# Kernel tuning notes

Measured on AMD Instinct MI355X. Metric: run time of the kernel, lower is better.

Reference implementation:

```python
import jax, jax.numpy as jnp
import numpy as np
import math

B, S, D, H = 4, 1024, 512, 8
HD = D // H
HID = 4 * D


def clinear(xr, xi, lm, ph, bm=None, bp=None):
    # magnitude-phase parameterized complex linear: W = exp(lm) * e^{i*ph}
    mag = jnp.exp(lm)
    wr = mag * jnp.cos(ph)
    wi = mag * jnp.sin(ph)
    r = xr @ wr.T - xi @ wi.T
    i = xr @ wi.T + xi @ wr.T
    if bm is not None:
        r = r + bm * jnp.cos(bp)
        i = i + bm * jnp.sin(bp)
    return r, i


def cln(xr, xi, gr, gi, br, bi, eps=1e-6):
    mr = xr.mean(-1, keepdims=True)
    mi = xi.mean(-1, keepdims=True)
    cr, ci = xr - mr, xi - mi
    var = (cr * cr + ci * ci).mean(-1, keepdims=True)
    inv = 1.0 / jnp.sqrt(var + eps)
    nr, ni = cr * inv, ci * inv
    return nr * gr - ni * gi + br, nr * gi + ni * gr + bi


def rotate_half(x):
    h = x.shape[-1] // 2
    return jnp.concatenate([-x[..., h:], x[..., :h]], axis=-1)


def split_heads(x):  # (B,S,D) -> (B,H,S,HD)
    return x.reshape(B, S, H, HD).transpose(0, 2, 1, 3)


def merge_heads(x):  # (B,H,S,HD) -> (B,S,D)
    return x.transpose(0, 2, 1, 3).reshape(B, S, D)


def setup_inputs() -> dict:
    key = jax.random.key(0)
    ks = iter(jax.random.split(key, 64))

    def lin(o_f, i_f):
        lm = jax.random.normal(next(ks), (o_f, i_f)) * 0.1 - 0.5 * math.log(i_f)
        ph = jax.random.uniform(next(ks), (o_f, i_f), minval=-math.pi, maxval=math.pi)
        return lm.astype(jnp.float32), ph.astype(jnp.float32)

    inp = {}
    inp['x_real'] = jax.random.normal(next(ks), (B, S, D), dtype=jnp.float32)
    inp['x_imag'] = jax.random.normal(next(ks), (B, S, D), dtype=jnp.float32)
    inp['ln1_gr'] = jnp.ones(D); inp['ln1_gi'] = jnp.zeros(D)
    inp['ln1_br'] = jnp.zeros(D); inp['ln1_bi'] = jnp.zeros(D)
    for nm in ['q', 'k', 'v', 'o']:
        lm, ph = lin(D, D)
        inp[nm + '_lm'] = lm; inp[nm + '_ph'] = ph
        inp[nm + '_bm'] = jnp.zeros(D); inp[nm + '_bp'] = jnp.zeros(D)
    inp['ln2_gr'] = jnp.ones(D); inp['ln2_gi'] = jnp.zeros(D)
    inp['ln2_br'] = jnp.zeros(D); inp['ln2_bi'] = jnp.zeros(D)
    inp['gate_lm'], inp['gate_ph'] = lin(HID, D)
    inp['up_lm'], inp['up_ph'] = lin(HID, D)
    inp['down_lm'], inp['down_ph'] = lin(D, HID)
    return inp


def reference(x_real, x_imag, ln1_gr, ln1_gi, ln1_br, ln1_bi,
              q_lm, q_ph, q_bm, q_bp, k_lm, k_ph, k_bm, k_bp,
              v_lm, v_ph, v_bm, v_bp, o_lm, o_ph, o_bm, o_bp,
              ln2_gr, ln2_gi, ln2_br, ln2_bi,
              gate_lm, gate_ph, up_lm, up_ph, down_lm, down_ph):
    # --- pre-attention complex LayerNorm ---
    hr, hi = cln(x_real, x_imag, ln1_gr, ln1_gi, ln1_br, ln1_bi)

    # --- complex QKV projections ---
    qr, qi = clinear(hr, hi, q_lm, q_ph, q_bm, q_bp)
    kr, ki = clinear(hr, hi, k_lm, k_ph, k_bm, k_bp)
    vr, vi = clinear(hr, hi, v_lm, v_ph, v_bm, v_bp)
    qr, qi = split_heads(qr), split_heads(qi)
    kr, ki = split_heads(kr), split_heads(ki)
    vr, vi = split_heads(vr), split_heads(vi)

    # --- complex RoPE (same real rotation applied to real & imag parts) ---
    pos = jnp.arange(S, dtype=jnp.float32)
    inv_freq = 1.0 / (10000.0 ** (jnp.arange(0, HD, 2, dtype=jnp.float32) / HD))
    freqs = pos[:, None] * inv_freq[None, :]          # (S, HD/2)
    cos = jnp.concatenate([jnp.cos(freqs)] * 2, -1)[None, None]  # (1,1,S,HD)
    sin = jnp.concatenate([jnp.sin(freqs)] * 2, -1)[None, None]
    rot = lambda x: x * cos + rotate_half(x) * sin
    qr, qi, kr, ki = rot(qr), rot(qi), rot(kr), rot(ki)

    # --- Hermitian attention: Re(q . conj(k)) = qr.kr + qi.ki ---
    scale = 1.0 / math.sqrt(HD)
    scores = (jnp.einsum('bhqd,bhkd->bhqk', qr, kr)
              + jnp.einsum('bhqd,bhkd->bhqk', qi, ki)) * scale
    causal = jnp.tril(jnp.ones((S, S), dtype=bool))
    scores = jnp.where(causal, scores, jnp.float32(-1e9))
    attn = jax.nn.softmax(scores, axis=-1)            # real-valued weights
    ar = jnp.einsum('bhqk,bhkd->bhqd', attn, vr)
    ai = jnp.einsum('bhqk,bhkd->bhqd', attn, vi)
    ar, ai = merge_heads(ar), merge_heads(ai)
    ar, ai = clinear(ar, ai, o_lm, o_ph, o_bm, o_bp)

    # --- residual + LN2 ---
    res_r, res_i = x_real + ar, x_imag + ai
    hr, hi = cln(res_r, res_i, ln2_gr, ln2_gi, ln2_br, ln2_bi)

    # --- complex gated FFN (SwiGLU-style, complex gating) ---
    gr_, gi_ = clinear(hr, hi, gate_lm, gate_ph)
    s = jax.nn.sigmoid(jnp.sqrt(gr_ * gr_ + gi_ * gi_))  # sigmoid(|gate|)
    gar, gai = gr_ * s, gi_ * s
    ur, ui = clinear(hr, hi, up_lm, up_ph)
    hid_r = gar * ur - gai * ui
    hid_i = gar * ui + gai * ur
    dr, di = clinear(hid_r, hid_i, down_lm, down_ph)

    out_r = res_r + dr
    out_i = res_i + di
    return jnp.stack([out_r, out_i], axis=0)  # (2, B, S, D)
```

## Files before the change

kernel.cpp:

```cpp
#include <hip/hip_runtime.h>
#include <math.h>

#define kB 4
#define kS 1024
#define kD 512
#define kH 8
#define kHD 64
#define kHID 2048
#define kNT (kB * kS)
#define kBSD (kNT * kD)

typedef __attribute__((ext_vector_type(8))) short bf16x8;
typedef __attribute__((ext_vector_type(4))) float f32x4;

#define AS1 __attribute__((address_space(1)))
#define AS3 __attribute__((address_space(3)))

__device__ __forceinline__ float bf2f(unsigned short u) {
  return __uint_as_float(((unsigned int)u) << 16);
}
__device__ __forceinline__ unsigned short f2bf(float f) {
  unsigned int u = __float_as_uint(f);
  u += 0x7fffu + ((u >> 16) & 1u);
  return (unsigned short)(u >> 16);
}
__device__ __forceinline__ unsigned int pack2(unsigned short a, unsigned short b) {
  return (unsigned)a | ((unsigned)b << 16);
}

#define BARC() do { asm volatile("" ::: "memory"); __builtin_amdgcn_s_barrier(); asm volatile("" ::: "memory"); } while (0)

__global__ __launch_bounds__(256) void build_wA_kernel(
    const float* __restrict__ qlm, const float* __restrict__ qph,
    const float* __restrict__ klm, const float* __restrict__ kph,
    const float* __restrict__ vlm, const float* __restrict__ vph,
    const float* __restrict__ olm, const float* __restrict__ oph,
    const float* __restrict__ qbm, const float* __restrict__ qbp,
    const float* __restrict__ kbm, const float* __restrict__ kbp,
    const float* __restrict__ vbm, const float* __restrict__ vbp,
    const float* __restrict__ obm, const float* __restrict__ obp,
    const float* __restrict__ xr, const float* __restrict__ xi,
    const float* __restrict__ g_r, const float* __restrict__ g_i,
    const float* __restrict__ b_r, const float* __restrict__ b_i,
    unsigned short* __restrict__ Wqkv, unsigned short* __restrict__ Wo,
    float* __restrict__ qkvBias, float* __restrict__ oBias,
    unsigned short* __restrict__ H) {
  int bx = blockIdx.x;
  if (bx >= 4104) {
    int w = threadIdx.x >> 6, lane = threadIdx.x & 63;
    int t = (bx - 4104) * 4 + w;
    int d0 = lane * 8;
    const float* xrt = xr + (size_t)t * 512 + d0;
    const float* xit = xi + (size_t)t * 512 + d0;
    float4 a0 = *(const float4*)&xrt[0];
    float4 a1 = *(const float4*)&xrt[4];
    float4 c0 = *(const float4*)&xit[0];
    float4 c1 = *(const float4*)&xit[4];
    float s1 = a0.x + a0.y + a0.z + a0.w + a1.x + a1.y + a1.z + a1.w;
    float s2 = c0.x + c0.y + c0.z + c0.w + c1.x + c1.y + c1.z + c1.w;
#pragma unroll
    for (int off = 1; off < 64; off <<= 1) {
      s1 += __shfl_xor(s1, off);
      s2 += __shfl_xor(s2, off);
    }
    float mr = s1 * (1.f / kD), mi = s2 * (1.f / kD);
    float ar[8] = {a0.x, a0.y, a0.z, a0.w, a1.x, a1.y, a1.z, a1.w};
    float ai[8] = {c0.x, c0.y, c0.z, c0.w, c1.x, c1.y, c1.z, c1.w};
    float v = 0.f;
#pragma unroll
    for (int e = 0; e < 8; e++) {
      float cr = ar[e] - mr, ci = ai[e] - mi;
      v += cr * cr + ci * ci;
    }
#pragma unroll
    for (int off = 1; off < 64; off <<= 1) v += __shfl_xor(v, off);
    float inv = rsqrtf(v * (1.f / kD) + 1e-6f);
    unsigned short pr[8], pi[8];
#pragma unroll
    for (int e = 0; e < 8; e++) {
      float nr = (ar[e] - mr) * inv;
      float ni = (ai[e] - mi) * inv;
      pr[e] = f2bf(nr * g_r[d0 + e] - ni * g_i[d0 + e] + b_r[d0 + e]);
      pi[e] = f2bf(nr * g_i[d0 + e] + ni * g_r[d0 + e] + b_i[d0 + e]);
    }
    unsigned short* ot = H + (size_t)t * 1024 + d0;
    *(bf16x8*)&ot[0] = *(const bf16x8*)pr;
    *(bf16x8*)&ot[512] = *(const bf16x8*)pi;
    return;
  }
  if (bx >= 4096) {
    int gid = (bx - 4096) * 256 + threadIdx.x;
    int seg = gid >> 9, m = gid & 511;
    const float* bm = seg == 0 ? qbm : seg == 1 ? kbm : seg == 2 ? vbm : obm;
    const float* bp = seg == 0 ? qbp : seg == 1 ? kbp : seg == 2 ? vbp : obp;
    float s, c;
    __sincosf(bp[m], &s, &c);
    float br = bm[m] * c, bi = bm[m] * s;
    if (seg < 3) {
      int h = m >> 6, d = m & 63;
      qkvBias[seg * 1024 + h * 128 + d] = br;
      qkvBias[seg * 1024 + h * 128 + 64 + d] = bi;
    } else {
      oBias[m] = br;
      oBias[512 + m] = bi;
    }
    return;
  }
  int gid = bx * 256 + threadIdx.x;
  int seg = gid >> 18;
  int id = gid & 262143;
  const float* lm = seg == 0 ? qlm : seg == 1 ? klm : seg == 2 ? vlm : olm;
  const float* ph = seg == 0 ? qph : seg == 1 ? kph : seg == 2 ? vph : oph;
  float mm = __expf(lm[id]);
  float s, c;
  __sincosf(ph[id], &s, &c);
  float wr = mm * c, wi = mm * s;
  int m = id >> 9, k = id & 511;
  if (seg < 3) {
    int h = m >> 6, d = m & 63;
    size_t rowR = (size_t)seg * 1024 + h * 128 + d;
    size_t rowI = rowR + 64;
    Wqkv[rowR * 1024 + k] = f2bf(wr);
    Wqkv[rowR * 1024 + 512 + k] = f2bf(-wi);
    Wqkv[rowI * 1024 + k] = f2bf(wi);
    Wqkv[rowI * 1024 + 512 + k] = f2bf(wr);
  } else {
    Wo[(size_t)m * 1024 + k] = f2bf(wr);
    Wo[(size_t)m * 1024 + 512 + k] = f2bf(-wi);
    Wo[(size_t)(512 + m) * 1024 + k] = f2bf(wi);
    Wo[(size_t)(512 + m) * 1024 + 512 + k] = f2bf(wr);
  }
}

__global__ __launch_bounds__(256) void build_wB_kernel(
    const float* __restrict__ glm, const float* __restrict__ gph,
    const float* __restrict__ ulm, const float* __restrict__ uph,
    const float* __restrict__ dlm, const float* __restrict__ dph,
    unsigned short* __restrict__ Wgu, unsigned short* __restrict__ Wd) {
  int gid = blockIdx.x * 256 + threadIdx.x;
  int seg = gid >> 19;
  int id0 = (gid & 524287) * 2;
  const float* lm = seg == 0 ? glm : seg == 1 ? ulm : dlm;
  const float* ph = seg == 0 ? gph : seg == 1 ? uph : dph;
  float2 lm2 = *(const float2*)&lm[id0];
  float2 ph2 = *(const float2*)&ph[id0];
  float m0 = __expf(lm2.x), m1 = __expf(lm2.y);
  float s0, c0, s1, c1;
  __sincosf(ph2.x, &s0, &c0);
  __sincosf(ph2.y, &s1, &c1);
  float wr0 = m0 * c0, wi0 = m0 * s0;
  float wr1 = m1 * c1, wi1 = m1 * s1;
  if (seg < 2) {
    int T = id0 >> 9, k = id0 & 511;
    size_t base = (size_t)(T >> 4) * 64 + (T & 15);
    size_t rR = base + (seg * 2 + 0) * 16;
    size_t rI = base + (seg * 2 + 1) * 16;
    *(unsigned int*)&Wgu[rR * 1024 + k] = pack2(f2bf(wr0), f2bf(wr1));
    *(unsigned int*)&Wgu[rR * 1024 + 512 + k] = pack2(f2bf(-wi0), f2bf(-wi1));
    *(unsigned int*)&Wgu[rI * 1024 + k] = pack2(f2bf(wi0), f2bf(wi1));
    *(unsigned int*)&Wgu[rI * 1024 + 512 + k] = pack2(f2bf(wr0), f2bf(wr1));
  } else {
    int m = id0 >> 11, j = id0 & 2047;
    ushort4 a;
    a.x = f2bf(wr0); a.y = f2bf(-wi0); a.z = f2bf(wr1); a.w = f2bf(-wi1);
    *(ushort4*)&Wd[(size_t)m * 4096 + 2 * j] = a;
    ushort4 b;
    b.x = f2bf(wi0); b.y = f2bf(wr0); b.z = f2bf(wi1); b.w = f2bf(wr1);
    *(ushort4*)&Wd[(size_t)(512 + m) * 4096 + 2 * j] = b;
  }
}

__global__ __launch_bounds__(256) void cln_kernel(
    const float* __restrict__ xr, const float* __restrict__ xi, int stride,
    const float* __restrict__ g_r, const float* __restrict__ g_i,
    const float* __restrict__ b_r, const float* __restrict__ b_i,
    unsigned short* __restrict__ out) {
  int w = threadIdx.x >> 6, lane = threadIdx.x & 63;
  int t = blockIdx.x * 4 + w;
  int d0 = lane * 8;
  const float* xrt = xr + (size_t)t * stride + d0;
  const float* xit = xi + (size_t)t * stride + d0;
  float4 a0 = *(const float4*)&xrt[0];
  float4 a1 = *(const float4*)&xrt[4];
  float4 c0 = *(const float4*)&xit[0];
  float4 c1 = *(const float4*)&xit[4];

  float s1 = a0.x + a0.y + a0.z + a0.w + a1.x + a1.y + a1.z + a1.w;
  float s2 = c0.x + c0.y + c0.z + c0.w + c1.x + c1.y + c1.z + c1.w;
#pragma unroll
  for (int off = 1; off < 64; off <<= 1) {
    s1 += __shfl_xor(s1, off);
    s2 += __shfl_xor(s2, off);
  }
  float mr = s1 * (1.f / kD), mi = s2 * (1.f / kD);

  float ar[8] = {a0.x, a0.y, a0.z, a0.w, a1.x, a1.y, a1.z, a1.w};
  float ai[8] = {c0.x, c0.y, c0.z, c0.w, c1.x, c1.y, c1.z, c1.w};
  float v = 0.f;
#pragma unroll
  for (int e = 0; e < 8; e++) {
    float cr = ar[e] - mr, ci = ai[e] - mi;
    v += cr * cr + ci * ci;
  }
#pragma unroll
  for (int off = 1; off < 64; off <<= 1) v += __shfl_xor(v, off);
  float inv = rsqrtf(v * (1.f / kD) + 1e-6f);

  unsigned short pr[8], pi[8];
#pragma unroll
  for (int e = 0; e < 8; e++) {
    float nr = (ar[e] - mr) * inv;
    float ni = (ai[e] - mi) * inv;
    pr[e] = f2bf(nr * g_r[d0 + e] - ni * g_i[d0 + e] + b_r[d0 + e]);
    pi[e] = f2bf(nr * g_i[d0 + e] + ni * g_r[d0 + e] + b_i[d0 + e]);
  }
  unsigned short* ot = out + (size_t)t * 1024 + d0;
  *(bf16x8*)&ot[0] = *(const bf16x8*)pr;
  *(bf16x8*)&ot[512] = *(const bf16x8*)pi;
}

__global__ __launch_bounds__(256) void cgemm_mfma_kernel(
    const unsigned short* __restrict__ X, int ldx,
    const unsigned short* __restrict__ Wt, int K,
    const float* __restrict__ bias, int mode,
    unsigned short* __restrict__ outb, int ldo,
    unsigned short* __restrict__ vtb) {
  __shared__ unsigned short Sh[128 * 64 * 2];
  unsigned short* Xs = Sh;
  unsigned short* Ws = Sh + 8192;

  const int tid = threadIdx.x;
  const int w = tid >> 6;
  const int lane = tid & 63;
  const int quad = lane >> 4;
  const int l15 = lane & 15;
  const int m0 = blockIdx.x * 128;
  const int n0 = blockIdx.y * 128;
  const int wm = (w & 1) * 64;
  const int wn = (w >> 1) * 64;

  const int rsub = lane >> 3;
  const int grow = w * 32 + rsub;
  const int gcol = ((lane & 7) ^ rsub) * 8;
  const unsigned short* gx = X + (size_t)(n0 + grow) * ldx + gcol;
  const unsigned short* gw = Wt + (size_t)(m0 + grow) * K + gcol;

  const int rg = (l15 & 7);

  f32x4 acc[4][4];
#pragma unroll
  for (int i = 0; i < 4; i++)
#pragma unroll
    for (int j = 0; j < 4; j++) acc[i][j] = (f32x4){0.f, 0.f, 0.f, 0.f};

  for (int k0 = 0; k0 < K; k0 += 64) {
    __syncthreads();
#pragma unroll
    for (int t = 0; t < 4; t++) {
      __builtin_amdgcn_global_load_lds((const AS1 void*)(gx + (size_t)t * 8 * ldx + k0),
                                       (AS3 void*)&Xs[w * 2048 + t * 512], 16, 0, 0);
      __builtin_amdgcn_global_load_lds((const AS1 void*)(gw + (size_t)t * 8 * K + k0),
                                       (AS3 void*)&Ws[w * 2048 + t * 512], 16, 0, 0);
    }
    __syncthreads();

#pragma unroll
    for (int ks = 0; ks < 2; ks++) {
      const int gsel = ((ks * 4 + quad) ^ rg) * 8;
      bf16x8 af[4], bf[4];
#pragma unroll
      for (int t = 0; t < 4; t++) {
        af[t] = *(const bf16x8*)&Xs[(wn + t * 16 + l15) * 64 + gsel];
        bf[t] = *(const bf16x8*)&Ws[(wm + t * 16 + l15) * 64 + gsel];
      }
#pragma unroll
      for (int i = 0; i < 4; i++)
#pragma unroll
        for (int j = 0; j < 4; j++)
          acc[i][j] = __builtin_amdgcn_mfma_f32_16x16x32_bf16(af[i], bf[j], acc[i][j], 0, 0, 0);
    }
  }

  if (mode == 4) {
    int T = ((m0 + wm) >> 6) * 16 + l15;
#pragma unroll
    for (int i = 0; i < 4; ++i) {
      int row0 = n0 + wn + i * 16 + quad * 4;
#pragma unroll
      for (int r = 0; r < 4; ++r) {
        float gr = acc[i][0][r], gi = acc[i][1][r];
        float ur = acc[i][2][r], ui = acc[i][3][r];
        float sg = __builtin_amdgcn_rcpf(1.f + __expf(-sqrtf(gr * gr + gi * gi)));
        float gar = gr * sg, gai = gi * sg;
        unsigned int pk = pack2(f2bf(gar * ur - gai * ui), f2bf(gar * ui + gai * ur));
        *(unsigned int*)&outb[(size_t)(row0 + r) * ldo + 2 * T] = pk;
      }
    }
  } else if (mode == 3 && m0 < 2048) {
#pragma unroll
    for (int j = 0; j < 4; ++j) {
      float bv = bias[m0 + wm + j * 16 + l15];
#pragma unroll
      for (int i = 0; i < 4; ++i)
#pragma unroll
        for (int r = 0; r < 4; ++r) acc[i][j][r] += bv;
    }
    const int sbase = ((n0 + wn) & (kS - 1)) + quad * 4;
#pragma unroll
    for (int j01 = 0; j01 < 2; ++j01) {
      float fi = (float)(j01 * 16 + l15);
      float f = __expf(fi * -0.28782313662425572f);
      float c1, s1, c16, s16, cI, sI;
      __sincosf(f, &s1, &c1);
      __sincosf(16.f * f, &s16, &c16);
      __sincosf((float)sbase * f, &sI, &cI);
#pragma unroll
      for (int i = 0; i < 4; ++i) {
        float cc = cI, ss = sI;
#pragma unroll
        for (int r = 0; r < 4; ++r) {
          float x0 = acc[i][j01][r], x1 = acc[i][j01 + 2][r];
          acc[i][j01][r] = x0 * cc - x1 * ss;
          acc[i][j01 + 2][r] = x1 * cc + x0 * ss;
          float cn = cc * c1 - ss * s1;
          ss = ss * c1 + cc * s1;
          cc = cn;
        }
        float cn = cI * c16 - sI * s16;
        sI = sI * c16 + cI * s16;
        cI = cn;
      }
    }
#pragma unroll
    for (int j = 0; j < 4; ++j) {
      int col = m0 + wm + j * 16 + l15;
#pragma unroll
      for (int i = 0; i < 4; ++i) {
        int row0 = n0 + wn + i * 16 + quad * 4;
#pragma unroll
        for (int r = 0; r < 4; ++r)
          outb[(size_t)(row0 + r) * ldo + col] = f2bf(acc[i][j][r]);
      }
    }
  } else {
    unsigned short* Ts = Sh;
#pragma unroll
    for (int p = 0; p < 2; ++p) {
      __syncthreads();
      if ((w & 1) == p) {
#pragma unroll
        for (int j = 0; j < 4; ++j) {
          float bv = bias[m0 + wm + j * 16 + l15];
          int fl = j * 16 + l15;
#pragma unroll
          for (int i = 0; i < 4; ++i) {
            int tk = wn + i * 16 + quad * 4;
#pragma unroll
            for (int r = 0; r < 4; ++r)
              Ts[fl * 130 + tk + r] = f2bf(acc[i][j][r] + bv);
          }
        }
      }
      __syncthreads();
      {
        int fr = tid >> 2, seg = tid & 3;
        int f = (m0 - 2048) + p * 64 + fr;
        int hh = f >> 7, dc = f & 127;
        int bb = n0 >> 10, sbase2 = (n0 & (kS - 1)) + seg * 32;
        unsigned short* dst = &vtb[(size_t)((bb * 8 + hh) * 128 + dc) * 1024 + sbase2];
        const unsigned short* src = &Ts[fr * 130 + seg * 32];
#pragma unroll
        for (int u = 0; u < 4; u++)
          *(bf16x8*)(dst + u * 8) = *(const bf16x8*)(src + u * 8);
      }
    }
  }
}

__global__ __launch_bounds__(512, 2) void cgemm_mfma_gu256_kernel(
    const unsigned short* __restrict__ X, int ldx,
    const unsigned short* __restrict__ Wt, int K,
    unsigned short* __restrict__ outb, int ldo) {
  __shared__ unsigned short Sh[65536];

  const int tid = threadIdx.x;
  const int w = tid >> 6;
  const int lane = tid & 63;
  const int quad = lane >> 4;
  const int l15 = lane & 15;
  const int m0 = blockIdx.x * 256;
  const int n0 = blockIdx.y * 256;
  const int wfeat = w & 1;
  const int wtok = w >> 1;

  const int srow = lane >> 3;
  const int sgran = ((lane & 7) ^ srow) * 8;
  const unsigned short* gA = X + (size_t)(n0 + w * 32 + srow) * ldx + sgran;
  const unsigned short* gB = Wt + (size_t)(m0 + w * 32 + srow) * K + sgran;

  f32x4 acc[4][8];
#pragma unroll
  for (int i = 0; i < 4; i++)
#pragma unroll
    for (int j = 0; j < 8; j++) acc[i][j] = (f32x4){0.f, 0.f, 0.f, 0.f};

  auto stage_tile = [&](int kt, int bsel) {
    const int k0 = kt * 64;
    unsigned short* dA = &Sh[bsel * 32768 + w * 2048];
    unsigned short* dB = &Sh[bsel * 32768 + 16384 + w * 2048];
#pragma unroll
    for (int u = 0; u < 4; ++u) {
      __builtin_amdgcn_global_load_lds((const AS1 void*)(gA + (size_t)u * 8 * ldx + k0),
                                       (AS3 void*)(dA + u * 512), 16, 0, 0);
      __builtin_amdgcn_global_load_lds((const AS1 void*)(gB + (size_t)u * 8 * K + k0),
                                       (AS3 void*)(dB + u * 512), 16, 0, 0);
    }
  };

  auto compute_tile = [&](const unsigned short* As, const unsigned short* Bs) {
    bf16x8 af[4][2];
#pragma unroll
    for (int i = 0; i < 4; ++i)
#pragma unroll
      for (int ks = 0; ks < 2; ++ks)
        af[i][ks] = *(const bf16x8*)&As[(wtok * 64 + i * 16 + l15) * 64 +
                                        (((ks * 4 + quad) ^ (l15 & 7)) * 8)];
#pragma unroll
    for (int jp = 0; jp < 4; ++jp) {
      bf16x8 bq[2][2];
#pragma unroll
      for (int jj = 0; jj < 2; ++jj)
#pragma unroll
        for (int ks = 0; ks < 2; ++ks)
          bq[jj][ks] = *(const bf16x8*)&Bs[(wfeat * 128 + (jp * 2 + jj) * 16 + l15) * 64 +
                                           (((ks * 4 + quad) ^ (l15 & 7)) * 8)];
      __builtin_amdgcn_s_setprio(1);
#pragma unroll
      for (int i = 0; i < 4; ++i)
#pragma unroll
        for (int jj = 0; jj < 2; ++jj) {
          const int j = jp * 2 + jj;
          acc[i][j] = __builtin_amdgcn_mfma_f32_16x16x32_bf16(af[i][0], bq[jj][0], acc[i][j], 0, 0, 0);
          acc[i][j] = __builtin_amdgcn_mfma_f32_16x16x32_bf16(af[i][1], bq[jj][1], acc[i][j], 0, 0, 0);
        }
      __builtin_amdgcn_s_setprio(0);
    }
  };

  const int nt = K >> 6;
  stage_tile(0, 0);
  for (int t = 0; t < nt; t += 2) {
    if (t + 1 < nt) {
      stage_tile(t + 1, 1);
      asm volatile("s_waitcnt vmcnt(8)" ::: "memory");
    } else {
      asm volatile("s_waitcnt vmcnt(0)" ::: "memory");
    }
    __builtin_amdgcn_s_barrier();
    asm volatile("" ::: "memory");
    compute_tile(&Sh[0], &Sh[16384]);
    asm volatile("" ::: "memory");
    __builtin_amdgcn_s_barrier();

    if (t + 2 < nt) {
      stage_tile(t + 2, 0);
      asm volatile("s_waitcnt vmcnt(8)" ::: "memory");
    } else {
      asm volatile("s_waitcnt vmcnt(0)" ::: "memory");
    }
    __builtin_amdgcn_s_barrier();
    asm volatile("" ::: "memory");
    compute_tile(&Sh[32768], &Sh[32768 + 16384]);
    asm volatile("" ::: "memory");
    __builtin_amdgcn_s_barrier();
  }

#pragma unroll
  for (int i = 0; i < 4; ++i) {
    int row0 = n0 + wtok * 64 + i * 16 + quad * 4;
#pragma unroll
    for (int jh = 0; jh < 2; ++jh) {
      int T = ((m0 + wfeat * 128 + jh * 64) >> 6) * 16 + l15;
#pragma unroll
      for (int r = 0; r < 4; ++r) {
        float gr = acc[i][jh * 4 + 0][r], gi = acc[i][jh * 4 + 1][r];
        float ur = acc[i][jh * 4 + 2][r], ui = acc[i][jh * 4 + 3][r];
        float sg = __builtin_amdgcn_rcpf(1.f + __expf(-sqrtf(gr * gr + gi * gi)));
        float gar = gr * sg, gai = gi * sg;
        unsigned int pk = pack2(f2bf(gar * ur - gai * ui), f2bf(gar * ui + gai * ur));
        *(unsigned int*)&outb[(size_t)(row0 + r) * ldo + 2 * T] = pk;
      }
    }
  }
}

__global__ __launch_bounds__(256) void cgemm_mfma_n64_kernel(
    const unsigned short* __restrict__ X, int ldx,
    const unsigned short* __restrict__ Wt, int K,
    const float* __restrict__ bias, int mode,
    const float* __restrict__ resr, const float* __restrict__ resi,
    float* __restrict__ outf) {
  __shared__ unsigned short Sh[24576];

  const int tid = threadIdx.x;
  const int w = tid >> 6;
  const int lane = tid & 63;
  const int quad = lane >> 4;
  const int l15 = lane & 15;
  const int m0 = blockIdx.x * 128;
  const int n0 = blockIdx.y * 64;
  const int wm = (w & 1) * 64;
  const int wn = (w >> 1) * 32;
  const int swz = l15 & 7;

  const int srow = lane >> 3;
  const int sgran = ((lane & 7) ^ srow) * 8;
  const unsigned short* gX = X + (size_t)(n0 + w * 16 + srow) * ldx + sgran;
  const unsigned short* gW = Wt + (size_t)(m0 + w * 32 + srow) * K + sgran;

  f32x4 acc[2][4];
#pragma unroll
  for (int i = 0; i < 2; i++)
#pragma unroll
    for (int j = 0; j < 4; j++) acc[i][j] = (f32x4){0.f, 0.f, 0.f, 0.f};

  auto stage_tile = [&](int kt, int bsel) {
    const int k0 = kt * 64;
    unsigned short* dX = &Sh[bsel * 12288 + w * 1024];
    unsigned short* dW = &Sh[bsel * 12288 + 4096 + w * 2048];
#pragma unroll
    for (int u = 0; u < 2; ++u)
      __builtin_amdgcn_global_load_lds((const AS1 void*)(gX + (size_t)u * 8 * ldx + k0),
                                       (AS3 void*)(dX + u * 512), 16, 0, 0);
#pragma unroll
    for (int u = 0; u < 4; ++u)
      __builtin_amdgcn_global_load_lds((const AS1 void*)(gW + (size_t)u * 8 * K + k0),
                                       (AS3 void*)(dW + u * 512), 16, 0, 0);
  };

  const int nt = K >> 6;
  stage_tile(0, 0);
  for (int t = 0; t < nt; ++t) {
    if (t + 1 < nt) {
      stage_tile(t + 1, (t + 1) & 1);
      asm volatile("s_waitcnt vmcnt(6)" ::: "memory");
    } else {
      asm volatile("s_waitcnt vmcnt(0)" ::: "memory");
    }
    BARC();
    const unsigned short* Xs = &Sh[(t & 1) * 12288];
    const unsigned short* Ws = &Sh[(t & 1) * 12288 + 4096];
#pragma unroll
    for (int ks = 0; ks < 2; ++ks) {
      const int gsel = ((ks * 4 + quad) ^ swz) * 8;
      bf16x8 af[2], bf[4];
#pragma unroll
      for (int t2 = 0; t2 < 2; ++t2)
        af[t2] = *(const bf16x8*)&Xs[(wn + t2 * 16 + l15) * 64 + gsel];
#pragma unroll
      for (int t2 = 0; t2 < 4; ++t2)
        bf[t2] = *(const bf16x8*)&Ws[(wm + t2 * 16 + l15) * 64 + gsel];
#pragma unroll
      for (int i = 0; i < 2; i++)
#pragma unroll
        for (int j = 0; j < 4; j++)
          acc[i][j] = __builtin_amdgcn_mfma_f32_16x16x32_bf16(af[i], bf[j], acc[i][j], 0, 0, 0);
    }
    BARC();
  }

#pragma unroll
  for (int j = 0; j < 4; ++j) {
    int col = m0 + wm + j * 16 + l15;
    float bv = bias ? bias[col] : 0.f;
#pragma unroll
    for (int i = 0; i < 2; ++i) {
      int row0 = n0 + wn + i * 16 + quad * 4;
#pragma unroll
      for (int r = 0; r < 4; ++r) {
        int row = row0 + r;
        float val = acc[i][j][r] + bv;
        if (mode == 1) {
          float xres = (col < 512) ? resr[(size_t)row * 512 + col]
                                   : resi[(size_t)row * 512 + col - 512];
          outf[(size_t)row * 1024 + col] = val + xres;
        } else {
          float rv = resr[(size_t)row * 1024 + col] + val;
          size_t dd = (col < 512) ? ((size_t)row * 512 + col)
                                  : ((size_t)kBSD + (size_t)row * 512 + (col - 512));
          outf[dd] = rv;
        }
      }
    }
  }
}

__global__ __launch_bounds__(256) void attn_mfma_kernel(
    const unsigned short* __restrict__ qkv,
    const unsigned short* __restrict__ vt,
    unsigned short* __restrict__ out) {
  __shared__ unsigned short Ks[64 * 136];
  __shared__ unsigned short Vs[128 * 72];
  __shared__ unsigned short Ps[4 * 16 * 72];

  const int tid = threadIdx.x;
  const int w = tid >> 6;
  const int lane = tid & 63;
  const int quad = lane >> 4;
  const int l15 = lane & 15;

  int bid = blockIdx.x;
  int second = bid >> 8;
  int u = bid & 255;
  int t_ = u & 15;
  const int qt = second ? (15 - t_) : t_;
  const int h = (u >> 4) & 7;
  const int b = second * 2 + (u >> 7);
  const int q0 = qt * 64;
  const int wrow0 = q0 + w * 16;

  bf16x8 qa[4];
  {
    size_t base = (size_t)(b * kS + wrow0 + l15) * 3072 + h * 128;
#pragma unroll
    for (int ks = 0; ks < 4; ks++)
      qa[ks] = *(const bf16x8*)&qkv[base + ks * 32 + quad * 8];
  }

  f32x4 oacc[8];
#pragma unroll
  for (int dt = 0; dt < 8; dt++) oacc[dt] = (f32x4){0.f, 0.f, 0.f, 0.f};
  float m_r[4] = {-1e30f, -1e30f, -1e30f, -1e30f};
  float l_r[4] = {0.f, 0.f, 0.f, 0.f};

  const int nkt = qt + 1;
  const float cexp = 0.1803368801f;

  const unsigned short* gkbase = qkv + 1024 + h * 128;
  const unsigned short* gvbase = vt + (size_t)((b * 8 + h) * 128) * 1024;

  for (int kt = 0; kt < nkt; ++kt) {
    const int k0 = kt * 64;
    __syncthreads();
    {
      const unsigned short* gk = gkbase + (size_t)(b * kS + k0) * 3072;
      int ch = tid * 4;
#pragma unroll
      for (int u2 = 0; u2 < 4; u2++) {
        int r = (ch + u2) >> 4, cc = ((ch + u2) & 15) * 8;
        *(bf16x8*)&Ks[r * 136 + cc] = *(const bf16x8*)&gk[(size_t)r * 3072 + cc];
      }
#pragma unroll
      for (int u2 = 0; u2 < 4; u2++) {
        int vr = (ch + u2) >> 3, vc = ((ch + u2) & 7) * 8;
        *(bf16x8*)&Vs[vr * 72 + vc] = *(const bf16x8*)&gvbase[(size_t)vr * 1024 + k0 + vc];
      }
    }
    __syncthreads();

    f32x4 s[4];
#pragma unroll
    for (int ns = 0; ns < 4; ns++) {
      s[ns] = (f32x4){0.f, 0.f, 0.f, 0.f};
#pragma unroll
      for (int ks = 0; ks < 4; ks++) {
        bf16x8 kb = *(const bf16x8*)&Ks[(ns * 16 + l15) * 136 + ks * 32 + quad * 8];
        s[ns] = __builtin_amdgcn_mfma_f32_16x16x32_bf16(qa[ks], kb, s[ns], 0, 0, 0);
      }
    }

    if (k0 + 63 > wrow0) {
#pragma unroll
      for (int r = 0; r < 4; r++) {
        int qrow = wrow0 + quad * 4 + r;
#pragma unroll
        for (int ns = 0; ns < 4; ns++)
          if (k0 + ns * 16 + l15 > qrow) s[ns][r] = -1e30f;
      }
    }

    float alpha[4];
#pragma unroll
    for (int r = 0; r < 4; r++) {
      float mx = fmaxf(fmaxf(s[0][r], s[1][r]), fmaxf(s[2][r], s[3][r]));
      mx = fmaxf(mx, __shfl_xor(mx, 1));
      mx = fmaxf(mx, __shfl_xor(mx, 2));
      mx = fmaxf(mx, __shfl_xor(mx, 4));
      mx = fmaxf(mx, __shfl_xor(mx, 8));
      float mn = fmaxf(m_r[r], mx);
      float al = exp2f((m_r[r] - mn) * cexp);
      m_r[r] = mn;
      float rs = 0.f;
#pragma unroll
      for (int ns = 0; ns < 4; ns++) {
        float p = exp2f((s[ns][r] - mn) * cexp);
        s[ns][r] = p;
        rs += p;
      }
      rs += __shfl_xor(rs, 1);
      rs += __shfl_xor(rs, 2);
      rs += __shfl_xor(rs, 4);
      rs += __shfl_xor(rs, 8);
      l_r[r] = l_r[r] * al + rs;
      alpha[r] = al;
    }

#pragma unroll
    for (int dt = 0; dt < 8; dt++)
#pragma unroll
      for (int r = 0; r < 4; r++) oacc[dt][r] *= alpha[r];

    unsigned short* pw = &Ps[w * 1152];
#pragma unroll
    for (int r = 0; r < 4; r++) {
      int q = quad * 4 + r;
#pragma unroll
      for (int ns = 0; ns < 4; ns++)
        pw[q * 72 + ns * 16 + l15] = f2bf(s[ns][r]);
    }
    bf16x8 pa0 = *(const bf16x8*)&pw[l15 * 72 + quad * 8];
    bf16x8 pa1 = *(const bf16x8*)&pw[l15 * 72 + 32 + quad * 8];

#pragma unroll
    for (int dt = 0; dt < 8; dt++) {
      bf16x8 vb0 = *(const bf16x8*)&Vs[(dt * 16 + l15) * 72 + quad * 8];
      bf16x8 vb1 = *(const bf16x8*)&Vs[(dt * 16 + l15) * 72 + 32 + quad * 8];
      oacc[dt] = __builtin_amdgcn_mfma_f32_16x16x32_bf16(pa0, vb0, oacc[dt], 0, 0, 0);
      oacc[dt] = __builtin_amdgcn_mfma_f32_16x16x32_bf16(pa1, vb1, oacc[dt], 0, 0, 0);
    }
  }

  float inv[4];
#pragma unroll
  for (int r = 0; r < 4; r++) inv[r] = __builtin_amdgcn_rcpf(l_r[r]);
#pragma unroll
  for (int dt = 0; dt < 8; dt++) {
    int dcat = dt * 16 + l15;
    int col = (dcat < 64) ? (h * 64 + dcat) : (512 + h * 64 + dcat - 64);
#pragma unroll
    for (int r = 0; r < 4; r++) {
      int tok = b * kS + wrow0 + quad * 4 + r;
      out[(size_t)tok * 1024 + col] = f2bf(oacc[dt][r] * inv[r]);
    }
  }
}

extern "C" void kernel_launch(void* const* d_in, const int* in_sizes, int n_in,
                              void* d_out, int out_size, void* d_ws, size_t ws_size,
                              hipStream_t stream) {
  const float* x_real = (const float*)d_in[0];
  const float* x_imag = (const float*)d_in[1];
  const float* ln1_gr = (const float*)d_in[2];
  const float* ln1_gi = (const float*)d_in[3];
  const float* ln1_br = (const float*)d_in[4];
  const float* ln1_bi = (const float*)d_in[5];
  const float* q_lm = (const float*)d_in[6];
  const float* q_ph = (const float*)d_in[7];
  const float* q_bm = (const float*)d_in[8];
  const float* q_bp = (const float*)d_in[9];
  const float* k_lm = (const float*)d_in[10];
  const float* k_ph = (const float*)d_in[11];
  const float* k_bm = (const float*)d_in[12];
  const float* k_bp = (const float*)d_in[13];
  const float* v_lm = (const float*)d_in[14];
  const float* v_ph = (const float*)d_in[15];
  const float* v_bm = (const float*)d_in[16];
  const float* v_bp = (const float*)d_in[17];
  const float* o_lm = (const float*)d_in[18];
  const float* o_ph = (const float*)d_in[19];
  const float* o_bm = (const float*)d_in[20];
  const float* o_bp = (const float*)d_in[21];
  const float* ln2_gr = (const float*)d_in[22];
  const float* ln2_gi = (const float*)d_in[23];
  const float* ln2_br = (const float*)d_in[24];
  const float* ln2_bi = (const float*)d_in[25];
  const float* gate_lm = (const float*)d_in[26];
  const float* gate_ph = (const float*)d_in[27];
  const float* up_lm = (const float*)d_in[28];
  const float* up_ph = (const float*)d_in[29];
  const float* down_lm = (const float*)d_in[30];
  const float* down_ph = (const float*)d_in[31];

  char* wsb = (char*)d_ws;
  unsigned short* Wqkv = (unsigned short*)(wsb + 0);
  unsigned short* Wo   = (unsigned short*)(wsb + 6291456);
  unsigned short* Wgu  = (unsigned short*)(wsb + 8388608);
  unsigned short* Wd   = (unsigned short*)(wsb + 25165824);
  float* qkvBias = (float*)(wsb + 33554432);
  float* oBias   = (float*)(wsb + 33566720);
  float* res     = (float*)(wsb + 33570816);
  unsigned short* H = (unsigned short*)(wsb + 50348032);
  char* big = wsb + 58736640;
  unsigned short* qkv     = (unsigned short*)big;
  unsigned short* attnout = (unsigned short*)(big + 25165824);
  unsigned short* vtb     = (unsigned short*)(big + 33554432);
  unsigned short* hid     = (unsigned short*)big;

  float* outf = (float*)d_out;

  build_wA_kernel<<<5128, 256, 0, stream>>>(q_lm, q_ph, k_lm, k_ph, v_lm, v_ph,
                                            o_lm, o_ph, q_bm, q_bp, k_bm, k_bp,
                                            v_bm, v_bp, o_bm, o_bp,
                                            x_real, x_imag, ln1_gr, ln1_gi,
                                            ln1_br, ln1_bi,
                                            Wqkv, Wo, qkvBias, oBias, H);
  build_wB_kernel<<<6144, 256, 0, stream>>>(gate_lm, gate_ph, up_lm, up_ph,
                                            down_lm, down_ph, Wgu, Wd);

  {
    dim3 g(3072 / 128, kNT / 128);
    cgemm_mfma_kernel<<<g, 256, 0, stream>>>(H, 1024, Wqkv, 1024, qkvBias, 3, qkv, 3072, vtb);
  }

  attn_mfma_kernel<<<kB * kH * (kS / 64), 256, 0, stream>>>(qkv, vtb, attnout);

  {
    dim3 g(1024 / 128, kNT / 64);
    cgemm_mfma_n64_kernel<<<g, 256, 0, stream>>>(attnout, 1024, Wo, 1024, oBias, 1,
                                                 x_real, x_imag, res);
  }

  cln_kernel<<<kNT / 4, 256, 0, stream>>>(res, res + 512, 1024, ln2_gr, ln2_gi, ln2_br, ln2_bi, H);

  {
    dim3 g(8192 / 256, kNT / 256);
    cgemm_mfma_gu256_kernel<<<g, 512, 0, stream>>>(H, 1024, Wgu, 1024, hid, 4096);
  }

  {
    dim3 g(1024 / 128, kNT / 64);
    cgemm_mfma_n64_kernel<<<g, 256, 0, stream>>>(hid, 4096, Wd, 4096, nullptr, 2,
                                                 res, nullptr, outf);
  }
}
```

Before: 388.3 us.

## Interleave chunked global-to-LDS staging with MFMA phases in gate/up GEMM

Restructures the gate/up fused GEMM main loop so that global_load_lds staging is split into four half-tile chunks. Each chunk is issued between LDS fragment reads and an MFMA quad, with barriers around each quad. The aim is to spread memory traffic across the compute phases and keep the next tiles in flight, so LDS refills overlap with MFMA work instead of arriving as one burst per tile. The cost is more barriers per k-tile and tighter vmcnt bookkeeping, which could serialize warps or create hazards if the counts are off.

```diff
diff --git a/kernel.cpp b/kernel.cpp
--- a/kernel.cpp
+++ b/kernel.cpp
@@ -392,11 +392,10 @@
   const int n0 = blockIdx.y * 256;
   const int wfeat = w & 1;
   const int wtok = w >> 1;
+  const int swz = l15 & 7;
 
   const int srow = lane >> 3;
   const int sgran = ((lane & 7) ^ srow) * 8;
-  const unsigned short* gA = X + (size_t)(n0 + w * 32 + srow) * ldx + sgran;
-  const unsigned short* gB = Wt + (size_t)(m0 + w * 32 + srow) * K + sgran;
 
   f32x4 acc[4][8];
 #pragma unroll
@@ -404,75 +403,90 @@
 #pragma unroll
     for (int j = 0; j < 8; j++) acc[i][j] = (f32x4){0.f, 0.f, 0.f, 0.f};
 
-  auto stage_tile = [&](int kt, int bsel) {
+  auto stage_chunk = [&](int kt, int which) {
     const int k0 = kt * 64;
-    unsigned short* dA = &Sh[bsel * 32768 + w * 2048];
-    unsigned short* dB = &Sh[bsel * 32768 + 16384 + w * 2048];
-#pragma unroll
-    for (int u = 0; u < 4; ++u) {
-      __builtin_amdgcn_global_load_lds((const AS1 void*)(gA + (size_t)u * 8 * ldx + k0),
-                                       (AS3 void*)(dA + u * 512), 16, 0, 0);
-      __builtin_amdgcn_global_load_lds((const AS1 void*)(gB + (size_t)u * 8 * K + k0),
-                                       (AS3 void*)(dB + u * 512), 16, 0, 0);
+    const int bsel = kt & 1;
+    const int half = which & 1;
+    if (which < 2) {
+      const unsigned short* g =
+          X + (size_t)(n0 + half * 128 + w * 16 + srow) * ldx + k0 + sgran;
+      unsigned short* d = &Sh[bsel * 32768 + (half * 128 + w * 16) * 64];
+#pragma unroll
+      for (int u = 0; u < 2; ++u)
+        __builtin_amdgcn_global_load_lds((const AS1 void*)(g + (size_t)u * 8 * ldx),
+                                         (AS3 void*)(d + u * 512), 16, 0, 0);
+    } else {
+      const unsigned short* g =
+          Wt + (size_t)(m0 + half * 128 + w * 16 + srow) * K + k0 + sgran;
+      unsigned short* d = &Sh[bsel * 32768 + 16384 + (half * 128 + w * 16) * 64];
+#pragma unroll
+      for (int u = 0; u < 2; ++u)
+        __builtin_amdgcn_global_load_lds((const AS1 void*)(g + (size_t)u * 8 * K),
+                                         (AS3 void*)(d + u * 512), 16, 0, 0);
     }
   };
 
-  auto compute_tile = [&](const unsigned short* As, const unsigned short* Bs) {
-    bf16x8 af[4][2];
+  bf16x8 af[4][2];
+  bf16x8 bq[4];
+
+  auto read_bq = [&](const unsigned short* Bs, int ks, int jh) {
+#pragma unroll
+    for (int jj = 0; jj < 4; ++jj)
+      bq[jj] = *(const bf16x8*)&Bs[(wfeat * 128 + jh * 64 + jj * 16 + l15) * 64 +
+                                   (((ks * 4 + quad) ^ swz) * 8)];
+  };
+
+  auto mfma_quad = [&](int ks, int jh) {
+    __builtin_amdgcn_s_barrier();
+    __builtin_amdgcn_s_setprio(1);
+#pragma unroll
+    for (int i = 0; i < 4; ++i)
+#pragma unroll
+      for (int jj = 0; jj < 4; ++jj)
+        acc[i][jh * 4 + jj] = __builtin_amdgcn_mfma_f32_16x16x32_bf16(
+            af[i][ks], bq[jj], acc[i][jh * 4 + jj], 0, 0, 0);
+    __builtin_amdgcn_s_setprio(0);
+    __builtin_amdgcn_s_barrier();
+  };
+
+  const int nt = K >> 6;
+  stage_chunk(0, 0); stage_chunk(0, 1); stage_chunk(0, 2); stage_chunk(0, 3);
+  stage_chunk(1, 0); stage_chunk(1, 1);
+  asm volatile("s_waitcnt vmcnt(4)" ::: "memory");
+  __builtin_amdgcn_s_barrier();
+
+  for (int t = 0; t < nt; ++t) {
+    const unsigned short* As = &Sh[(t & 1) * 32768];
+    const unsigned short* Bs = &Sh[(t & 1) * 32768 + 16384];
+
 #pragma unroll
     for (int i = 0; i < 4; ++i)
 #pragma unroll
       for (int ks = 0; ks < 2; ++ks)
         af[i][ks] = *(const bf16x8*)&As[(wtok * 64 + i * 16 + l15) * 64 +
-                                        (((ks * 4 + quad) ^ (l15 & 7)) * 8)];
-#pragma unroll
-    for (int jp = 0; jp < 4; ++jp) {
-      bf16x8 bq[2][2];
-#pragma unroll
-      for (int jj = 0; jj < 2; ++jj)
-#pragma unroll
-        for (int ks = 0; ks < 2; ++ks)
-          bq[jj][ks] = *(const bf16x8*)&Bs[(wfeat * 128 + (jp * 2 + jj) * 16 + l15) * 64 +
-                                           (((ks * 4 + quad) ^ (l15 & 7)) * 8)];
-      __builtin_amdgcn_s_setprio(1);
-#pragma unroll
-      for (int i = 0; i < 4; ++i)
-#pragma unroll
-        for (int jj = 0; jj < 2; ++jj) {
-          const int j = jp * 2 + jj;
-          acc[i][j] = __builtin_amdgcn_mfma_f32_16x16x32_bf16(af[i][0], bq[jj][0], acc[i][j], 0, 0, 0);
-          acc[i][j] = __builtin_amdgcn_mfma_f32_16x16x32_bf16(af[i][1], bq[jj][1], acc[i][j], 0, 0, 0);
-        }
-      __builtin_amdgcn_s_setprio(0);
-    }
-  };
-
-  const int nt = K >> 6;
-  stage_tile(0, 0);
-  for (int t = 0; t < nt; t += 2) {
-    if (t + 1 < nt) {
-      stage_tile(t + 1, 1);
-      asm volatile("s_waitcnt vmcnt(8)" ::: "memory");
+                                        (((ks * 4 + quad) ^ swz) * 8)];
+    read_bq(Bs, 0, 0);
+    if (t + 1 < nt) stage_chunk(t + 1, 2);
+    mfma_quad(0, 0);
+#pragma unroll
+    for (int i = 0; i < 4; ++i) asm volatile("" :: "v"(af[i][1]));
+
+    read_bq(Bs, 0, 1);
+    if (t + 1 < nt) stage_chunk(t + 1, 3);
+    mfma_quad(0, 1);
+
+    read_bq(Bs, 1, 0);
+    if (t + 2 < nt) stage_chunk(t + 2, 0);
+    mfma_quad(1, 0);
+
+    read_bq(Bs, 1, 1);
+    if (t + 2 < nt) {
+      stage_chunk(t + 2, 1);
+      asm volatile("s_waitcnt vmcnt(4)" ::: "memory");
     } else {
       asm volatile("s_waitcnt vmcnt(0)" ::: "memory");
     }
-    __builtin_amdgcn_s_barrier();
-    asm volatile("" ::: "memory");
-    compute_tile(&Sh[0], &Sh[16384]);
-    asm volatile("" ::: "memory");
-    __builtin_amdgcn_s_barrier();
-
-    if (t + 2 < nt) {
-      stage_tile(t + 2, 0);
-      asm volatile("s_waitcnt vmcnt(8)" ::: "memory");
-    } else {
-      asm volatile("s_waitcnt vmcnt(0)" ::: "memory");
-    }
-    __builtin_amdgcn_s_barrier();
-    asm volatile("" ::: "memory");
-    compute_tile(&Sh[32768], &Sh[32768 + 16384]);
-    asm volatile("" ::: "memory");
-    __builtin_amdgcn_s_barrier();
+    mfma_quad(1, 1);
   }
 
 #pragma unroll
```

Result: no change. 385.7 us (-0.7%).

## Shrink gate/up GEMM tile to 256x128 with BK=32 and higher occupancy

Applied to the files above, without the earlier changes.

The fused gate/up complex GEMM moves from a 256x256 tile with K-step 64 and two-tile unrolled double buffering to a 256x128 tile with K-step 32, single-iteration ping-pong buffering and a new XOR swizzle. LDS use drops from 128KB to 48KB and launch bounds ask for 4 blocks per CU, doubling the grid. This aims at better occupancy and latency hiding, at the cost of less operand reuse per tile, more barriers per unit of K, and more redundant loads of X.

```diff
diff --git a/kernel.cpp b/kernel.cpp
--- a/kernel.cpp
+++ b/kernel.cpp
@@ -377,119 +377,89 @@
   }
 }
 
-__global__ __launch_bounds__(512, 2) void cgemm_mfma_gu256_kernel(
+__global__ __launch_bounds__(512, 4) void cgemm_mfma_gu256_kernel(
     const unsigned short* __restrict__ X, int ldx,
     const unsigned short* __restrict__ Wt, int K,
     unsigned short* __restrict__ outb, int ldo) {
-  __shared__ unsigned short Sh[65536];
+  __shared__ unsigned short Sh[24576];
 
   const int tid = threadIdx.x;
   const int w = tid >> 6;
   const int lane = tid & 63;
   const int quad = lane >> 4;
   const int l15 = lane & 15;
-  const int m0 = blockIdx.x * 256;
+  const int m0 = blockIdx.x * 128;
   const int n0 = blockIdx.y * 256;
   const int wfeat = w & 1;
   const int wtok = w >> 1;
 
-  const int srow = lane >> 3;
-  const int sgran = ((lane & 7) ^ srow) * 8;
-  const unsigned short* gA = X + (size_t)(n0 + w * 32 + srow) * ldx + sgran;
-  const unsigned short* gB = Wt + (size_t)(m0 + w * 32 + srow) * K + sgran;
-
-  f32x4 acc[4][8];
+  const int srow = lane >> 2;
+  const int sgran = ((lane & 3) ^ ((srow >> 1) & 3)) * 8;
+  const unsigned short* gX = X + (size_t)(n0 + w * 32 + srow) * ldx + sgran;
+  const unsigned short* gW = Wt + (size_t)(m0 + w * 16 + srow) * K + sgran;
+
+  f32x4 acc[4][4];
 #pragma unroll
   for (int i = 0; i < 4; i++)
 #pragma unroll
-    for (int j = 0; j < 8; j++) acc[i][j] = (f32x4){0.f, 0.f, 0.f, 0.f};
+    for (int j = 0; j < 4; j++) acc[i][j] = (f32x4){0.f, 0.f, 0.f, 0.f};
 
   auto stage_tile = [&](int kt, int bsel) {
-    const int k0 = kt * 64;
-    unsigned short* dA = &Sh[bsel * 32768 + w * 2048];
-    unsigned short* dB = &Sh[bsel * 32768 + 16384 + w * 2048];
-#pragma unroll
-    for (int u = 0; u < 4; ++u) {
-      __builtin_amdgcn_global_load_lds((const AS1 void*)(gA + (size_t)u * 8 * ldx + k0),
-                                       (AS3 void*)(dA + u * 512), 16, 0, 0);
-      __builtin_amdgcn_global_load_lds((const AS1 void*)(gB + (size_t)u * 8 * K + k0),
-                                       (AS3 void*)(dB + u * 512), 16, 0, 0);
-    }
+    const int k0 = kt * 32;
+    unsigned short* dX = &Sh[bsel * 12288 + w * 1024];
+    unsigned short* dW = &Sh[bsel * 12288 + 8192 + w * 512];
+    __builtin_amdgcn_global_load_lds((const AS1 void*)(gX + k0),
+                                     (AS3 void*)(dX), 16, 0, 0);
+    __builtin_amdgcn_global_load_lds((const AS1 void*)(gX + (size_t)16 * ldx + k0),
+                                     (AS3 void*)(dX + 512), 16, 0, 0);
+    __builtin_amdgcn_global_load_lds((const AS1 void*)(gW + k0),
+                                     (AS3 void*)(dW), 16, 0, 0);
   };
 
-  auto compute_tile = [&](const unsigned short* As, const unsigned short* Bs) {
-    bf16x8 af[4][2];
-#pragma unroll
-    for (int i = 0; i < 4; ++i)
-#pragma unroll
-      for (int ks = 0; ks < 2; ++ks)
-        af[i][ks] = *(const bf16x8*)&As[(wtok * 64 + i * 16 + l15) * 64 +
-                                        (((ks * 4 + quad) ^ (l15 & 7)) * 8)];
-#pragma unroll
-    for (int jp = 0; jp < 4; ++jp) {
-      bf16x8 bq[2][2];
-#pragma unroll
-      for (int jj = 0; jj < 2; ++jj)
-#pragma unroll
-        for (int ks = 0; ks < 2; ++ks)
-          bq[jj][ks] = *(const bf16x8*)&Bs[(wfeat * 128 + (jp * 2 + jj) * 16 + l15) * 64 +
-                                           (((ks * 4 + quad) ^ (l15 & 7)) * 8)];
-      __builtin_amdgcn_s_setprio(1);
-#pragma unroll
-      for (int i = 0; i < 4; ++i)
-#pragma unroll
-        for (int jj = 0; jj < 2; ++jj) {
-          const int j = jp * 2 + jj;
-          acc[i][j] = __builtin_amdgcn_mfma_f32_16x16x32_bf16(af[i][0], bq[jj][0], acc[i][j], 0, 0, 0);
-          acc[i][j] = __builtin_amdgcn_mfma_f32_16x16x32_bf16(af[i][1], bq[jj][1], acc[i][j], 0, 0, 0);
-        }
-      __builtin_amdgcn_s_setprio(0);
-    }
-  };
-
-  const int nt = K >> 6;
+  const int gsel = ((quad ^ ((l15 >> 1) & 3)) * 8);
+  const int aoff = (wtok * 64 + l15) * 32 + gsel;
+  const int boff = (wfeat * 64 + l15) * 32 + gsel;
+
+  const int nt = K >> 5;
   stage_tile(0, 0);
-  for (int t = 0; t < nt; t += 2) {
+  for (int t = 0; t < nt; ++t) {
     if (t + 1 < nt) {
-      stage_tile(t + 1, 1);
-      asm volatile("s_waitcnt vmcnt(8)" ::: "memory");
+      stage_tile(t + 1, (t + 1) & 1);
+      asm volatile("s_waitcnt vmcnt(3)" ::: "memory");
     } else {
       asm volatile("s_waitcnt vmcnt(0)" ::: "memory");
     }
-    __builtin_amdgcn_s_barrier();
-    asm volatile("" ::: "memory");
-    compute_tile(&Sh[0], &Sh[16384]);
-    asm volatile("" ::: "memory");
-    __builtin_amdgcn_s_barrier();
-
-    if (t + 2 < nt) {
-      stage_tile(t + 2, 0);
-      asm volatile("s_waitcnt vmcnt(8)" ::: "memory");
-    } else {
-      asm volatile("s_waitcnt vmcnt(0)" ::: "memory");
-    }
-    __builtin_amdgcn_s_barrier();
-    asm volatile("" ::: "memory");
-    compute_tile(&Sh[32768], &Sh[32768 + 16384]);
-    asm volatile("" ::: "memory");
-    __builtin_amdgcn_s_barrier();
-  }
-
+    BARC();
+    const unsigned short* As = &Sh[(t & 1) * 12288];
+    const unsigned short* Ws = &Sh[(t & 1) * 12288 + 8192];
+    bf16x8 af[4];
+#pragma unroll
+    for (int i = 0; i < 4; ++i)
+      af[i] = *(const bf16x8*)&As[aoff + i * 512];
+    __builtin_amdgcn_s_setprio(1);
+#pragma unroll
+    for (int j = 0; j < 4; ++j) {
+      bf16x8 bq = *(const bf16x8*)&Ws[boff + j * 512];
+#pragma unroll
+      for (int i = 0; i < 4; ++i)
+        acc[i][j] = __builtin_amdgcn_mfma_f32_16x16x32_bf16(af[i], bq, acc[i][j], 0, 0, 0);
+    }
+    __builtin_amdgcn_s_setprio(0);
+    BARC();
+  }
+
+  const int T = ((m0 + wfeat * 64) >> 6) * 16 + l15;
 #pragma unroll
   for (int i = 0; i < 4; ++i) {
     int row0 = n0 + wtok * 64 + i * 16 + quad * 4;
 #pragma unroll
-    for (int jh = 0; jh < 2; ++jh) {
-      int T = ((m0 + wfeat * 128 + jh * 64) >> 6) * 16 + l15;
-#pragma unroll
-      for (int r = 0; r < 4; ++r) {
-        float gr = acc[i][jh * 4 + 0][r], gi = acc[i][jh * 4 + 1][r];
-        float ur = acc[i][jh * 4 + 2][r], ui = acc[i][jh * 4 + 3][r];
-        float sg = __builtin_amdgcn_rcpf(1.f + __expf(-sqrtf(gr * gr + gi * gi)));
-        float gar = gr * sg, gai = gi * sg;
-        unsigned int pk = pack2(f2bf(gar * ur - gai * ui), f2bf(gar * ui + gai * ur));
-        *(unsigned int*)&outb[(size_t)(row0 + r) * ldo + 2 * T] = pk;
-      }
+    for (int r = 0; r < 4; ++r) {
+      float gr = acc[i][0][r], gi = acc[i][1][r];
+      float ur = acc[i][2][r], ui = acc[i][3][r];
+      float sg = __builtin_amdgcn_rcpf(1.f + __expf(-sqrtf(gr * gr + gi * gi)));
+      float gar = gr * sg, gai = gi * sg;
+      unsigned int pk = pack2(f2bf(gar * ur - gai * ui), f2bf(gar * ui + gai * ur));
+      *(unsigned int*)&outb[(size_t)(row0 + r) * ldo + 2 * T] = pk;
     }
   }
 }
@@ -823,7 +793,7 @@
   cln_kernel<<<kNT / 4, 256, 0, stream>>>(res, res + 512, 1024, ln2_gr, ln2_gi, ln2_br, ln2_bi, H);
 
   {
-    dim3 g(8192 / 256, kNT / 256);
+    dim3 g(8192 / 128, kNT / 256);
     cgemm_mfma_gu256_kernel<<<g, 512, 0, stream>>>(H, 1024, Wgu, 1024, hid, 4096);
   }
 
```

Result: slower. 398.0 us (+2.5%).
